# Kernel optimization log

Hardware: AMD Instinct MI355X
Metric: run time of the kernel (lower is better)

## Reference

```python
import jax, jax.numpy as jnp
import numpy as np

IN_F = 1280
OUT_F = 1280
RANK = 4
NUM_LORAS = 50
LORA_STRIDE = 4
SCALE = 1.0


def setup_inputs() -> dict:
    key = jax.random.key(0)
    k1, k2, k3, k4, k5 = jax.random.split(key, 5)
    x = jax.random.normal(k1, (16, 4096, IN_F), dtype=jnp.float32)
    lora_id = jax.random.randint(k2, (16,), 0, 200)  # raw ids; divided by stride in forward
    W = jax.random.normal(k3, (OUT_F, IN_F), dtype=jnp.float32) * 0.02  # base linear (bias=False)
    # lora_down init: normal(std=1/r); lora_up is zero-init in source but we use small
    # random values so the LoRA path is numerically exercised.
    Wd = jax.random.normal(k4, (NUM_LORAS, RANK, IN_F), dtype=jnp.float32) * (1.0 / RANK)
    Wu = jax.random.normal(k5, (NUM_LORAS, OUT_F, RANK), dtype=jnp.float32) * 0.02
    return {"x": x, "lora_id": lora_id, "W": W, "Wd": Wd, "Wu": Wu}


def reference(x, lora_id, W, Wd, Wu):
    # x: [G, T, D_in]; one chunk per lora_id entry (chunk size 1 along batch).
    idx = lora_id // LORA_STRIDE            # [G] lora index per chunk
    active = lora_id >= 0                   # chunks with negative id skip LoRA
    safe_idx = jnp.where(active, idx, 0)

    base = jnp.einsum('btd,od->bto', x, W)  # dense base linear, shared weight
    # per-chunk gathered low-rank path (dropout is identity in eval mode)
    down = jnp.einsum('btd,brd->btr', x, Wd[safe_idx])   # [G, T, r]
    up = jnp.einsum('btr,bor->bto', down, Wu[safe_idx])  # [G, T, D_out]
    return base + jnp.where(active[:, None, None], up * SCALE, jnp.zeros((), x.dtype))
```

## Files before the change

### kernel.cpp

```cpp
#include <hip/hip_runtime.h>
#include <hip/hip_bf16.h>

typedef __attribute__((ext_vector_type(8))) short short8;
typedef __attribute__((ext_vector_type(4))) short short4v;
typedef __attribute__((ext_vector_type(4))) float f32x4;

#define D_IN 1280
#define D_OUT 1280
#define RANK 4
#define LORA_STRIDE 4
#define BM 128
#define BN 128
#define BK 64
#define NK (D_IN / BK)

__device__ __forceinline__ short f2bs(float f) {
    __hip_bfloat16 h = __float2bfloat16(f);
    return __builtin_bit_cast(short, h);
}

__device__ __forceinline__ int swz(int row, int k) {
    return row * BK + ((((k >> 3) ^ row) & 7) << 3) + (k & 7);
}

__global__ __launch_bounds__(256, 2)
void lora_fused_gemm_db(const float* __restrict__ x,
                        const int* __restrict__ lora_id,
                        const float* __restrict__ W,
                        const float* __restrict__ Wd,
                        const float* __restrict__ Wu,
                        float* __restrict__ out,
                        int t_len, int ntiles_n) {
    __shared__ short sA[2][BM * BK];
    __shared__ short sB[2][BN * BK];

    const int tid = threadIdx.x;

    const int nwg = gridDim.x;
    const int cpx = nwg >> 3;
    const int bsw = (blockIdx.x & 7) * cpx + (blockIdx.x >> 3);
    const int ntile = bsw % ntiles_n;
    const int mtile = bsw / ntiles_n;
    const int gm = mtile * BM;
    const int gn = ntile * BN;

    const int chunk = gm / t_len;
    const int lid_raw = lora_id[chunk];
    const bool active = lid_raw >= 0;
    const int idx = active ? (lid_raw / LORA_STRIDE) : 0;
    const float lscale = active ? 1.0f : 0.0f;

    const int arow = tid >> 1;
    const int acol = (tid & 1) * 32;
    const float* xp = x + (long)(gm + arow) * D_IN + acol;

    const int kg = tid & 15;
    const int nr = tid >> 4;
    const float* wp = W + (long)gn * D_IN + kg * 4;
    const float* wdp = Wd + (long)idx * RANK * D_IN + kg * 4;

    f32x4 u[8];
    #pragma unroll
    for (int s = 0; s < 8; ++s) {
        f32x4 t = *reinterpret_cast<const f32x4*>(
            Wu + ((long)idx * D_OUT + gn + nr + 16 * s) * RANK);
        #pragma unroll
        for (int j = 0; j < 4; ++j) u[s][j] = t[j] * lscale;
    }

    const int wave = tid >> 6;
    const int lane = tid & 63;
    const int wm = (wave & 1) * 64;
    const int wn = (wave >> 1) * 64;
    const int quad = lane >> 4;
    const int lr = lane & 15;

    f32x4 acc[4][4];
    #pragma unroll
    for (int a = 0; a < 4; ++a)
        #pragma unroll
        for (int b = 0; b < 4; ++b)
            #pragma unroll
            for (int j = 0; j < 4; ++j) acc[a][b][j] = 0.f;

    f32x4 xv[8], wd[RANK], wv[8];

    #pragma unroll
    for (int q = 0; q < 8; ++q)
        xv[q] = *reinterpret_cast<const f32x4*>(xp + q * 4);
    #pragma unroll
    for (int r = 0; r < RANK; ++r)
        wd[r] = *reinterpret_cast<const f32x4*>(wdp + (long)r * D_IN);
    #pragma unroll
    for (int s = 0; s < 8; ++s)
        wv[s] = *reinterpret_cast<const f32x4*>(wp + (long)(nr + 16 * s) * D_IN);

    #pragma unroll
    for (int q = 0; q < 4; ++q) {
        short8 v;
        #pragma unroll
        for (int j = 0; j < 4; ++j) {
            v[j]     = f2bs(xv[2 * q][j]);
            v[j + 4] = f2bs(xv[2 * q + 1][j]);
        }
        *reinterpret_cast<short8*>(&sA[0][swz(arow, acol + q * 8)]) = v;
    }
    #pragma unroll
    for (int s = 0; s < 8; ++s) {
        const int n = nr + 16 * s;
        short4v e;
        #pragma unroll
        for (int j = 0; j < 4; ++j) {
            float v = wv[s][j] + u[s][0] * wd[0][j] + u[s][1] * wd[1][j]
                               + u[s][2] * wd[2][j] + u[s][3] * wd[3][j];
            e[j] = f2bs(v);
        }
        *reinterpret_cast<short4v*>(&sB[0][swz(n, kg * 4)]) = e;
    }

    int cur = 0;
    for (int kt = 0; kt < NK; ++kt) {
        __syncthreads();

        const bool more = (kt + 1) < NK;
        if (more) {
            const int kn = (kt + 1) * BK;
            #pragma unroll
            for (int q = 0; q < 8; ++q)
                xv[q] = *reinterpret_cast<const f32x4*>(xp + kn + q * 4);
            #pragma unroll
            for (int r = 0; r < RANK; ++r)
                wd[r] = *reinterpret_cast<const f32x4*>(wdp + (long)r * D_IN + kn);
            #pragma unroll
            for (int s = 0; s < 8; ++s)
                wv[s] = *reinterpret_cast<const f32x4*>(
                    wp + (long)(nr + 16 * s) * D_IN + kn);
        }

        const short* cA = sA[cur];
        const short* cB = sB[cur];
        #pragma unroll
        for (int ks = 0; ks < 2; ++ks) {
            short8 af[4], bfr[4];
            #pragma unroll
            for (int mi = 0; mi < 4; ++mi)
                af[mi] = *reinterpret_cast<const short8*>(
                    &cA[swz(wm + mi * 16 + lr, ks * 32 + quad * 8)]);
            #pragma unroll
            for (int ni = 0; ni < 4; ++ni)
                bfr[ni] = *reinterpret_cast<const short8*>(
                    &cB[swz(wn + ni * 16 + lr, ks * 32 + quad * 8)]);
            #pragma unroll
            for (int mi = 0; mi < 4; ++mi)
                #pragma unroll
                for (int ni = 0; ni < 4; ++ni)
                    acc[mi][ni] = __builtin_amdgcn_mfma_f32_16x16x32_bf16(
                        af[mi], bfr[ni], acc[mi][ni], 0, 0, 0);
        }

        if (more) {
            short* nA = sA[cur ^ 1];
            short* nB = sB[cur ^ 1];
            #pragma unroll
            for (int q = 0; q < 4; ++q) {
                short8 v;
                #pragma unroll
                for (int j = 0; j < 4; ++j) {
                    v[j]     = f2bs(xv[2 * q][j]);
                    v[j + 4] = f2bs(xv[2 * q + 1][j]);
                }
                *reinterpret_cast<short8*>(&nA[swz(arow, acol + q * 8)]) = v;
            }
            #pragma unroll
            for (int s = 0; s < 8; ++s) {
                const int n = nr + 16 * s;
                short4v e;
                #pragma unroll
                for (int j = 0; j < 4; ++j) {
                    float v = wv[s][j] + u[s][0] * wd[0][j] + u[s][1] * wd[1][j]
                                       + u[s][2] * wd[2][j] + u[s][3] * wd[3][j];
                    e[j] = f2bs(v);
                }
                *reinterpret_cast<short4v*>(&nB[swz(n, kg * 4)]) = e;
            }
        }
        cur ^= 1;
    }

    #pragma unroll
    for (int mi = 0; mi < 4; ++mi) {
        #pragma unroll
        for (int ni = 0; ni < 4; ++ni) {
            float* op = out + (long)(gm + wm + mi * 16 + quad * 4) * D_OUT
                            + gn + wn + ni * 16 + lr;
            #pragma unroll
            for (int j = 0; j < 4; ++j) op[(long)j * D_OUT] = acc[mi][ni][j];
        }
    }
}

__global__ __launch_bounds__(256, 2)
void lora_fused_gemm_fb(const float* __restrict__ x,
                        const int* __restrict__ lora_id,
                        const float* __restrict__ W,
                        const float* __restrict__ Wd,
                        const float* __restrict__ Wu,
                        float* __restrict__ out,
                        int t_len, int ntiles_n) {
    __shared__ short sA[BM * BK];
    __shared__ short sB[BN * BK];

    const int tid = threadIdx.x;
    const int bx = blockIdx.x;
    const int ntile = bx % ntiles_n;
    const int mtile = bx / ntiles_n;
    const int gm = mtile * BM;
    const int gn = ntile * BN;

    const int chunk = gm / t_len;
    const int lid_raw = lora_id[chunk];
    const bool active = lid_raw >= 0;
    const int idx = active ? (lid_raw / LORA_STRIDE) : 0;
    const float lscale = active ? 1.0f : 0.0f;

    const int arow = tid >> 1;
    const int acol = (tid & 1) * 32;
    const float* xp = x + (long)(gm + arow) * D_IN + acol;

    const int kg = tid & 15;
    const int nr = tid >> 4;
    const float* wp = W + (long)gn * D_IN + kg * 4;
    const float* wdp = Wd + (long)idx * RANK * D_IN + kg * 4;

    f32x4 u[8];
    #pragma unroll
    for (int s = 0; s < 8; ++s) {
        f32x4 t = *reinterpret_cast<const f32x4*>(
            Wu + ((long)idx * D_OUT + gn + nr + 16 * s) * RANK);
        #pragma unroll
        for (int j = 0; j < 4; ++j) u[s][j] = t[j] * lscale;
    }

    const int wave = tid >> 6;
    const int lane = tid & 63;
    const int wm = (wave & 1) * 64;
    const int wn = (wave >> 1) * 64;
    const int quad = lane >> 4;
    const int lr = lane & 15;

    f32x4 acc[4][4];
    #pragma unroll
    for (int a = 0; a < 4; ++a)
        #pragma unroll
        for (int b = 0; b < 4; ++b)
            #pragma unroll
            for (int j = 0; j < 4; ++j) acc[a][b][j] = 0.f;

    for (int k0 = 0; k0 < D_IN; k0 += BK) {
        if (k0) __syncthreads();

        f32x4 xv[8];
        #pragma unroll
        for (int q = 0; q < 8; ++q)
            xv[q] = *reinterpret_cast<const f32x4*>(xp + k0 + q * 4);
        #pragma unroll
        for (int q = 0; q < 4; ++q) {
            short8 v;
            #pragma unroll
            for (int j = 0; j < 4; ++j) {
                v[j]     = f2bs(xv[2 * q][j]);
                v[j + 4] = f2bs(xv[2 * q + 1][j]);
            }
            *reinterpret_cast<short8*>(&sA[swz(arow, acol + q * 8)]) = v;
        }

        f32x4 wd[RANK];
        #pragma unroll
        for (int r = 0; r < RANK; ++r)
            wd[r] = *reinterpret_cast<const f32x4*>(wdp + (long)r * D_IN + k0);
        #pragma unroll
        for (int s = 0; s < 8; ++s) {
            const int n = nr + 16 * s;
            f32x4 wv = *reinterpret_cast<const f32x4*>(wp + (long)n * D_IN + k0);
            short4v e;
            #pragma unroll
            for (int j = 0; j < 4; ++j) {
                float v = wv[j] + u[s][0] * wd[0][j] + u[s][1] * wd[1][j]
                                + u[s][2] * wd[2][j] + u[s][3] * wd[3][j];
                e[j] = f2bs(v);
            }
            *reinterpret_cast<short4v*>(&sB[swz(n, kg * 4)]) = e;
        }

        __syncthreads();

        #pragma unroll
        for (int ks = 0; ks < 2; ++ks) {
            short8 af[4], bfr[4];
            #pragma unroll
            for (int mi = 0; mi < 4; ++mi)
                af[mi] = *reinterpret_cast<const short8*>(
                    &sA[swz(wm + mi * 16 + lr, ks * 32 + quad * 8)]);
            #pragma unroll
            for (int ni = 0; ni < 4; ++ni)
                bfr[ni] = *reinterpret_cast<const short8*>(
                    &sB[swz(wn + ni * 16 + lr, ks * 32 + quad * 8)]);
            #pragma unroll
            for (int mi = 0; mi < 4; ++mi)
                #pragma unroll
                for (int ni = 0; ni < 4; ++ni)
                    acc[mi][ni] = __builtin_amdgcn_mfma_f32_16x16x32_bf16(
                        af[mi], bfr[ni], acc[mi][ni], 0, 0, 0);
        }
    }

    #pragma unroll
    for (int mi = 0; mi < 4; ++mi) {
        #pragma unroll
        for (int ni = 0; ni < 4; ++ni) {
            float* op = out + (long)(gm + wm + mi * 16 + quad * 4) * D_OUT
                            + gn + wn + ni * 16 + lr;
            #pragma unroll
            for (int j = 0; j < 4; ++j) op[(long)j * D_OUT] = acc[mi][ni][j];
        }
    }
}

extern "C" void kernel_launch(void* const* d_in, const int* in_sizes, int n_in,
                              void* d_out, int out_size, void* d_ws, size_t ws_size,
                              hipStream_t stream) {
    const float* x   = (const float*)d_in[0];
    const int* lid   = (const int*)d_in[1];
    const float* W   = (const float*)d_in[2];
    const float* Wd  = (const float*)d_in[3];
    const float* Wu  = (const float*)d_in[4];
    float* out       = (float*)d_out;

    const int M = in_sizes[0] / D_IN;
    const int G = in_sizes[1];
    const int t_len = M / G;
    const int ntiles_n = D_OUT / BN;
    const int nblocks = (M / BM) * ntiles_n;

    if (M % BM == 0 && t_len % BM == 0 && (nblocks & 7) == 0) {
        lora_fused_gemm_db<<<nblocks, 256, 0, stream>>>(
            x, lid, W, Wd, Wu, out, t_len, ntiles_n);
    } else {
        lora_fused_gemm_fb<<<nblocks, 256, 0, stream>>>(
            x, lid, W, Wd, Wu, out, t_len, ntiles_n);
    }
}
```

Baseline: 1.080 ms.

## Compute LoRA down-projection via extra MFMA and apply up-projection in epilogue

Instead of folding the rank-4 LoRA update into each B tile (W + Wu·Wd) during every K-step, the kernel now loads plain W into shared memory. It computes x·Wdᵀ with one extra MFMA per M-subtile, reading Wd straight from global memory. The up-projection is then applied in the epilogue via lane shuffles and FMAs. This removes the per-element rank-4 FMAs and Wd loads from the B staging path, but adds extra MFMAs, per-iteration global loads of Wd inside the compute loop, and bf16 rounding of the down-projection intermediate.

```diff
diff --git a/kernel.cpp b/kernel.cpp
--- a/kernel.cpp
+++ b/kernel.cpp
@@ -24,13 +24,13 @@
 }
 
 __global__ __launch_bounds__(256, 2)
-void lora_fused_gemm_db(const float* __restrict__ x,
-                        const int* __restrict__ lora_id,
-                        const float* __restrict__ W,
-                        const float* __restrict__ Wd,
-                        const float* __restrict__ Wu,
-                        float* __restrict__ out,
-                        int t_len, int ntiles_n) {
+void lora_gemm_mfma(const float* __restrict__ x,
+                    const int* __restrict__ lora_id,
+                    const float* __restrict__ W,
+                    const float* __restrict__ Wd,
+                    const float* __restrict__ Wu,
+                    float* __restrict__ out,
+                    int t_len, int ntiles_n) {
     __shared__ short sA[2][BM * BK];
     __shared__ short sB[2][BN * BK];
 
@@ -57,16 +57,6 @@
     const int kg = tid & 15;
     const int nr = tid >> 4;
     const float* wp = W + (long)gn * D_IN + kg * 4;
-    const float* wdp = Wd + (long)idx * RANK * D_IN + kg * 4;
-
-    f32x4 u[8];
-    #pragma unroll
-    for (int s = 0; s < 8; ++s) {
-        f32x4 t = *reinterpret_cast<const f32x4*>(
-            Wu + ((long)idx * D_OUT + gn + nr + 16 * s) * RANK);
-        #pragma unroll
-        for (int j = 0; j < 4; ++j) u[s][j] = t[j] * lscale;
-    }
 
     const int wave = tid >> 6;
     const int lane = tid & 63;
@@ -75,22 +65,34 @@
     const int quad = lane >> 4;
     const int lr = lane & 15;
 
+    const float* wdl = Wd + ((long)idx * RANK + (lr & 3)) * D_IN;
+
+    f32x4 uw[4];
+    #pragma unroll
+    for (int ni = 0; ni < 4; ++ni) {
+        f32x4 t = *reinterpret_cast<const f32x4*>(
+            Wu + ((long)idx * D_OUT + gn + wn + ni * 16 + lr) * RANK);
+        #pragma unroll
+        for (int j = 0; j < 4; ++j) uw[ni][j] = t[j] * lscale;
+    }
+
     f32x4 acc[4][4];
-    #pragma unroll
-    for (int a = 0; a < 4; ++a)
+    f32x4 acc_d[4];
+    #pragma unroll
+    for (int a = 0; a < 4; ++a) {
+        #pragma unroll
+        for (int j = 0; j < 4; ++j) acc_d[a][j] = 0.f;
         #pragma unroll
         for (int b = 0; b < 4; ++b)
             #pragma unroll
             for (int j = 0; j < 4; ++j) acc[a][b][j] = 0.f;
-
-    f32x4 xv[8], wd[RANK], wv[8];
+    }
+
+    f32x4 xv[8], wv[8];
 
     #pragma unroll
     for (int q = 0; q < 8; ++q)
         xv[q] = *reinterpret_cast<const f32x4*>(xp + q * 4);
-    #pragma unroll
-    for (int r = 0; r < RANK; ++r)
-        wd[r] = *reinterpret_cast<const f32x4*>(wdp + (long)r * D_IN);
     #pragma unroll
     for (int s = 0; s < 8; ++s)
         wv[s] = *reinterpret_cast<const f32x4*>(wp + (long)(nr + 16 * s) * D_IN);
@@ -107,15 +109,10 @@
     }
     #pragma unroll
     for (int s = 0; s < 8; ++s) {
-        const int n = nr + 16 * s;
         short4v e;
         #pragma unroll
-        for (int j = 0; j < 4; ++j) {
-            float v = wv[s][j] + u[s][0] * wd[0][j] + u[s][1] * wd[1][j]
-                               + u[s][2] * wd[2][j] + u[s][3] * wd[3][j];
-            e[j] = f2bs(v);
-        }
-        *reinterpret_cast<short4v*>(&sB[0][swz(n, kg * 4)]) = e;
+        for (int j = 0; j < 4; ++j) e[j] = f2bs(wv[s][j]);
+        *reinterpret_cast<short4v*>(&sB[0][swz(nr + 16 * s, kg * 4)]) = e;
     }
 
     int cur = 0;
@@ -129,9 +126,6 @@
             for (int q = 0; q < 8; ++q)
                 xv[q] = *reinterpret_cast<const f32x4*>(xp + kn + q * 4);
             #pragma unroll
-            for (int r = 0; r < RANK; ++r)
-                wd[r] = *reinterpret_cast<const f32x4*>(wdp + (long)r * D_IN + kn);
-            #pragma unroll
             for (int s = 0; s < 8; ++s)
                 wv[s] = *reinterpret_cast<const f32x4*>(
                     wp + (long)(nr + 16 * s) * D_IN + kn);
@@ -141,6 +135,11 @@
         const short* cB = sB[cur];
         #pragma unroll
         for (int ks = 0; ks < 2; ++ks) {
+            f32x4 d0 = *reinterpret_cast<const f32x4*>(
+                wdl + kt * BK + ks * 32 + quad * 8);
+            f32x4 d1 = *reinterpret_cast<const f32x4*>(
+                wdl + kt * BK + ks * 32 + quad * 8 + 4);
+
             short8 af[4], bfr[4];
             #pragma unroll
             for (int mi = 0; mi < 4; ++mi)
@@ -150,12 +149,24 @@
             for (int ni = 0; ni < 4; ++ni)
                 bfr[ni] = *reinterpret_cast<const short8*>(
                     &cB[swz(wn + ni * 16 + lr, ks * 32 + quad * 8)]);
+
             #pragma unroll
             for (int mi = 0; mi < 4; ++mi)
                 #pragma unroll
                 for (int ni = 0; ni < 4; ++ni)
                     acc[mi][ni] = __builtin_amdgcn_mfma_f32_16x16x32_bf16(
                         af[mi], bfr[ni], acc[mi][ni], 0, 0, 0);
+
+            short8 df;
+            #pragma unroll
+            for (int j = 0; j < 4; ++j) {
+                df[j]     = f2bs(d0[j]);
+                df[j + 4] = f2bs(d1[j]);
+            }
+            #pragma unroll
+            for (int mi = 0; mi < 4; ++mi)
+                acc_d[mi] = __builtin_amdgcn_mfma_f32_16x16x32_bf16(
+                    af[mi], df, acc_d[mi], 0, 0, 0);
         }
 
         if (more) {
@@ -173,15 +184,10 @@
             }
             #pragma unroll
             for (int s = 0; s < 8; ++s) {
-                const int n = nr + 16 * s;
                 short4v e;
                 #pragma unroll
-                for (int j = 0; j < 4; ++j) {
-                    float v = wv[s][j] + u[s][0] * wd[0][j] + u[s][1] * wd[1][j]
-                                       + u[s][2] * wd[2][j] + u[s][3] * wd[3][j];
-                    e[j] = f2bs(v);
-                }
-                *reinterpret_cast<short4v*>(&nB[swz(n, kg * 4)]) = e;
+                for (int j = 0; j < 4; ++j) e[j] = f2bs(wv[s][j]);
+                *reinterpret_cast<short4v*>(&nB[swz(nr + 16 * s, kg * 4)]) = e;
             }
         }
         cur ^= 1;
@@ -189,12 +195,23 @@
 
     #pragma unroll
     for (int mi = 0; mi < 4; ++mi) {
+        float dm[4][4];
+        #pragma unroll
+        for (int r = 0; r < 4; ++r)
+            #pragma unroll
+            for (int j = 0; j < 4; ++j)
+                dm[r][j] = __shfl(acc_d[mi][j], (lane & 48) + r);
         #pragma unroll
         for (int ni = 0; ni < 4; ++ni) {
             float* op = out + (long)(gm + wm + mi * 16 + quad * 4) * D_OUT
                             + gn + wn + ni * 16 + lr;
             #pragma unroll
-            for (int j = 0; j < 4; ++j) op[(long)j * D_OUT] = acc[mi][ni][j];
+            for (int j = 0; j < 4; ++j) {
+                float v = acc[mi][ni][j]
+                        + dm[0][j] * uw[ni][0] + dm[1][j] * uw[ni][1]
+                        + dm[2][j] * uw[ni][2] + dm[3][j] * uw[ni][3];
+                op[(long)j * D_OUT] = v;
+            }
         }
     }
 }
@@ -343,7 +360,7 @@
     const int nblocks = (M / BM) * ntiles_n;
 
     if (M % BM == 0 && t_len % BM == 0 && (nblocks & 7) == 0) {
-        lora_fused_gemm_db<<<nblocks, 256, 0, stream>>>(
+        lora_gemm_mfma<<<nblocks, 256, 0, stream>>>(
             x, lid, W, Wd, Wu, out, t_len, ntiles_n);
     } else {
         lora_fused_gemm_fb<<<nblocks, 256, 0, stream>>>(
```

New measurement: 1.178 ms. 9.0% more time.
